# Optimization experiments

Hardware: AMD Instinct MI355X
Metric: run time of the kernel (lower is better)

Reference implementation:

```python
import jax, jax.numpy as jnp
import numpy as np

B, N, DIM, H, DH = 2, 2048, 1024, 16, 64
INNER = H * DH
ROPE_BASE = 10000.0


def setup_inputs() -> dict:
    key = jax.random.key(0)
    ks = jax.random.split(key, 6)
    s = 0.02
    return {
        "x": jax.random.normal(ks[0], (B, N, DIM), jnp.float32),
        "Wq": jax.random.normal(ks[1], (DIM, INNER), jnp.float32) * s,
        "Wk": jax.random.normal(ks[2], (DIM, INNER), jnp.float32) * s,
        "Wv": jax.random.normal(ks[3], (DIM, INNER), jnp.float32) * s,
        "Wo": jax.random.normal(ks[4], (INNER, DIM), jnp.float32) * s,
        "bo": jnp.zeros((DIM,), jnp.float32),
    }


def _rotate_half(x):
    # einops '... (d r) -> ... d r' with r=2: x1 = even lanes, x2 = odd lanes,
    # then cat((-x2, x1), dim=-1)
    x1 = x[..., 0::2]
    x2 = x[..., 1::2]
    return jnp.concatenate([-x2, x1], axis=-1)


def _rope_sin_cos(n, d, dtype):
    # inv_freq over arange(0, d, 2); emb = cat(f, f) -> length d
    inv_freq = 1.0 / (ROPE_BASE ** (jnp.arange(0, d, 2, dtype=jnp.float32) / d))
    f = jnp.arange(n, dtype=jnp.float32)[:, None] * inv_freq[None, :]  # [n, d/2]
    e = jnp.concatenate([f, f], axis=-1)  # [n, d]
    return jnp.sin(e).astype(dtype), jnp.cos(e).astype(dtype)


def _apply_rope(t, sin, cos):
    # t: [b, h, n, d]; sin/cos: [n, d]; rot_dim == d (full head), t_pass empty
    return t * cos[None, None] + _rotate_half(t) * sin[None, None]


def reference(x, Wq, Wk, Wv, Wo, bo):
    b, n, _ = x.shape
    scale = DH ** (-0.5)

    def split_heads(y):  # [b, n, h*d] -> [b, h, n, d]
        return y.reshape(b, n, H, DH).transpose(0, 2, 1, 3)

    q = split_heads(x @ Wq)
    k = split_heads(x @ Wk)
    v = split_heads(x @ Wv)

    sin, cos = _rope_sin_cos(n, DH, x.dtype)
    q = _apply_rope(q, sin, cos)
    k = _apply_rope(k, sin, cos)

    # causal SDPA (mask=None path -> is_causal=True), eval mode so dropout_p=0
    scores = jnp.einsum("bhqd,bhkd->bhqk", q, k) * scale
    causal = jnp.tril(jnp.ones((n, n), dtype=bool))
    scores = jnp.where(causal[None, None], scores, jnp.finfo(scores.dtype).min)
    probs = jax.nn.softmax(scores, axis=-1)
    attn = jnp.einsum("bhqk,bhkd->bhqd", probs, v)

    out = attn.transpose(0, 2, 1, 3).reshape(b, n, INNER) @ Wo + bo
    return out, k, v
```

## Files before the change

kernel.cpp:

```cpp
#include <hip/hip_runtime.h>
#include <cstdint>
#include <cmath>

#define BB   2
#define NN   2048
#define DIMM 1024
#define NHH  16
#define DHH  64
#define MMR  (BB * NN)

typedef _Float16 half8  __attribute__((ext_vector_type(8)));
typedef _Float16 half4v __attribute__((ext_vector_type(4)));
typedef float    f32x4  __attribute__((ext_vector_type(4)));

#define GLD16(gp, lp)                                                          \
  __builtin_amdgcn_global_load_lds(                                            \
      (const __attribute__((address_space(1))) unsigned int*)(gp),             \
      (__attribute__((address_space(3))) unsigned int*)(lp), 16, 0, 0)

__global__ __launch_bounds__(256) void cvt_x_kernel(const float* __restrict__ x,
                                                    _Float16* __restrict__ xh) {
  int i = (blockIdx.x * 256 + threadIdx.x) * 4;
  float4 v = *(const float4*)(x + i);
  half4v h;
  h[0] = (_Float16)v.x; h[1] = (_Float16)v.y;
  h[2] = (_Float16)v.z; h[3] = (_Float16)v.w;
  *(half4v*)(xh + i) = h;
}

__global__ __launch_bounds__(256) void transpose_w_kernel(
    const float* __restrict__ Wq, const float* __restrict__ Wk,
    const float* __restrict__ Wv, const float* __restrict__ Wo,
    _Float16* __restrict__ wt) {
  __shared__ float tile[64][65];
  int z = blockIdx.z;
  const float* W = (z == 0) ? Wq : (z == 1) ? Wk : (z == 2) ? Wv : Wo;
  _Float16* dst = wt + (size_t)z * 1024 * 1024;
  int r0 = blockIdx.x * 64;
  int c0 = blockIdx.y * 64;
  int t = threadIdx.x;
  int tr = t >> 4;
  int tc = (t & 15) * 4;
#pragma unroll
  for (int i = 0; i < 4; ++i) {
    float4 v = *(const float4*)(W + (size_t)(r0 + tr + i * 16) * 1024 + c0 + tc);
    tile[tr + i * 16][tc + 0] = v.x;
    tile[tr + i * 16][tc + 1] = v.y;
    tile[tr + i * 16][tc + 2] = v.z;
    tile[tr + i * 16][tc + 3] = v.w;
  }
  __syncthreads();
#pragma unroll
  for (int i = 0; i < 4; ++i) {
    int nl = tr + i * 16;
    half4v hv;
    hv[0] = (_Float16)tile[tc + 0][nl];
    hv[1] = (_Float16)tile[tc + 1][nl];
    hv[2] = (_Float16)tile[tc + 2][nl];
    hv[3] = (_Float16)tile[tc + 3][nl];
    *(half4v*)(dst + (size_t)(c0 + nl) * 1024 + r0 + tc) = hv;
  }
}

__global__ __launch_bounds__(256) void gemm_qkv_kernel(
    const _Float16* __restrict__ xh, const _Float16* __restrict__ wt,
    float* __restrict__ ko, float* __restrict__ vo,
    _Float16* __restrict__ qh, _Float16* __restrict__ kh,
    _Float16* __restrict__ vth) {
  __shared__ __align__(16) char smem[49152];
  _Float16* As = (_Float16*)smem;
  _Float16* Bs = (_Float16*)(smem + 24576);
  float (*Cs)[65] = (float(*)[65])smem;

  const int m0  = blockIdx.x * 64;
  const int ngl = blockIdx.y * 64;
  const int mat = ngl >> 10;
  const int n0  = ngl & 1023;
  const _Float16* wb = wt + (size_t)mat * 1024 * 1024;
  const int t = threadIdx.x;
  const int wv = t >> 6, lane = t & 63, l16 = lane & 15, quad = lane >> 4;
  const int r  = t >> 3;
  const int cl = t & 7;
  const int csw = (cl ^ (r & 7)) * 8;
  const _Float16* pa0 = xh + (size_t)(m0 + r) * 1024 + csw;
  const _Float16* pa1 = pa0 + 32 * 1024;
  const _Float16* pb0 = wb + (size_t)(n0 + r) * 1024 + csw;
  const _Float16* pb1 = pb0 + 32 * 1024;
  f32x4 acc[4] = {};
  const int arow = wv * 16 + l16;
  const int a7 = arow & 7;

#define STAGE_AB(k0s, nb) do {                                                 \
    GLD16(pa0 + (k0s), As + (nb) * 4096 + wv * 512);                           \
    GLD16(pa1 + (k0s), As + (nb) * 4096 + 2048 + wv * 512);                    \
    GLD16(pb0 + (k0s), Bs + (nb) * 4096 + wv * 512);                           \
    GLD16(pb1 + (k0s), Bs + (nb) * 4096 + 2048 + wv * 512);                    \
  } while (0)

  STAGE_AB(0, 0);
  STAGE_AB(64, 1);
  int cur = 0;
  for (int k0 = 0; k0 < 1024; k0 += 64) {
    if (k0 + 128 < 1024) {
      int nb = cur + 2; if (nb >= 3) nb -= 3;
      STAGE_AB(k0 + 128, nb);
      asm volatile("s_waitcnt vmcnt(8)" ::: "memory");
    } else if (k0 + 64 < 1024) {
      asm volatile("s_waitcnt vmcnt(4)" ::: "memory");
    } else {
      asm volatile("s_waitcnt vmcnt(0)" ::: "memory");
    }
    __builtin_amdgcn_s_barrier();
    asm volatile("" ::: "memory");
    const _Float16* Ab = As + cur * 4096;
    const _Float16* Bb = Bs + cur * 4096;
    half8 af0 = *(const half8*)(Ab + arow * 64 + (quad ^ a7) * 8);
    half8 af1 = *(const half8*)(Ab + arow * 64 + ((4 + quad) ^ a7) * 8);
#pragma unroll
    for (int nt = 0; nt < 4; ++nt) {
      int brow = nt * 16 + l16;
      int b7 = brow & 7;
      half8 bf0 = *(const half8*)(Bb + brow * 64 + (quad ^ b7) * 8);
      half8 bf1 = *(const half8*)(Bb + brow * 64 + ((4 + quad) ^ b7) * 8);
      acc[nt] = __builtin_amdgcn_mfma_f32_16x16x32_f16(af0, bf0, acc[nt], 0, 0, 0);
      acc[nt] = __builtin_amdgcn_mfma_f32_16x16x32_f16(af1, bf1, acc[nt], 0, 0, 0);
    }
    asm volatile("s_waitcnt lgkmcnt(0)" ::: "memory");
    __builtin_amdgcn_s_barrier();
    asm volatile("" ::: "memory");
    cur = (cur == 2) ? 0 : cur + 1;
  }
#undef STAGE_AB
#pragma unroll
  for (int nt = 0; nt < 4; ++nt)
#pragma unroll
    for (int rr = 0; rr < 4; ++rr)
      Cs[wv * 16 + quad * 4 + rr][nt * 16 + l16] = acc[nt][rr];
  __syncthreads();
  int lr = t >> 2;
  int cseg = (t & 3) * 16;
  int m = m0 + lr;
  int b = m >> 11;
  int pos = m & 2047;
  int h = n0 >> 6;
  int bhh = b * NHH + h;
  float vals[16];
  if (mat == 2) {
#pragma unroll
    for (int j = 0; j < 16; ++j) vals[j] = Cs[lr][cseg + j];
  } else {
    float fpos = (float)pos;
#pragma unroll
    for (int j = 0; j < 16; ++j) {
      int i = cseg + j;
      int jd = (i < 32) ? i : (i - 32);
      float invf = exp2f((float)jd * -0.41524101186092029f);
      float ang = fpos * invf;
      float sv, cv;
      sincosf(ang, &sv, &cv);
      float partner = (i < 32) ? -Cs[lr][2 * i + 1] : Cs[lr][2 * (i - 32)];
      vals[j] = Cs[lr][i] * cv + partner * sv;
    }
  }
  size_t rowb = ((size_t)bhh * NN + pos) * DHH + cseg;
  if (mat == 0) {
    half8 h0, h1;
#pragma unroll
    for (int j = 0; j < 8; ++j) { h0[j] = (_Float16)(vals[j] * 0.125f); h1[j] = (_Float16)(vals[8 + j] * 0.125f); }
    *(half8*)(qh + rowb) = h0;
    *(half8*)(qh + rowb + 8) = h1;
  } else if (mat == 1) {
#pragma unroll
    for (int j4 = 0; j4 < 4; ++j4) {
      float4 o;
      o.x = vals[j4 * 4 + 0]; o.y = vals[j4 * 4 + 1];
      o.z = vals[j4 * 4 + 2]; o.w = vals[j4 * 4 + 3];
      *(float4*)(ko + rowb + j4 * 4) = o;
    }
    half8 h0, h1;
#pragma unroll
    for (int j = 0; j < 8; ++j) { h0[j] = (_Float16)vals[j]; h1[j] = (_Float16)vals[8 + j]; }
    *(half8*)(kh + rowb) = h0;
    *(half8*)(kh + rowb + 8) = h1;
  } else {
#pragma unroll
    for (int j4 = 0; j4 < 4; ++j4) {
      float4 o;
      o.x = vals[j4 * 4 + 0]; o.y = vals[j4 * 4 + 1];
      o.z = vals[j4 * 4 + 2]; o.w = vals[j4 * 4 + 3];
      *(float4*)(vo + rowb + j4 * 4) = o;
    }
#pragma unroll
    for (int j = 0; j < 16; ++j)
      vth[((size_t)bhh * DHH + cseg + j) * NN + pos] = (_Float16)vals[j];
  }
}

__global__ __launch_bounds__(512) void fattn_kernel(
    const _Float16* __restrict__ qh, const _Float16* __restrict__ kh,
    const _Float16* __restrict__ vth, _Float16* __restrict__ ah) {
  __shared__ __align__(16) _Float16 Kt[3][4096];
  __shared__ __align__(16) _Float16 Vt[3][4096];
  __shared__ __align__(16) _Float16 Pb[8][16][72];
  const int lin  = (int)blockIdx.x;
  const int xcd  = lin & 7;
  const int slot = lin >> 3;
  const int bh   = xcd * 4 + (slot & 3);
  const int pair = slot >> 2;
  const int t = threadIdx.x;
  const int wv = t >> 6, lane = t & 63, l16 = lane & 15, quad = lane >> 4;
  const int b = bh >> 4, h = bh & 15;
  const _Float16* kg = kh + (size_t)bh * NN * DHH;
  const _Float16* vg = vth + (size_t)bh * DHH * NN;
  const int srow = t >> 3;
  const int sc   = ((t & 7) ^ (srow & 7)) * 8;
  half8 ones;
#pragma unroll
  for (int j = 0; j < 8; ++j) ones[j] = (_Float16)1.f;

#define STAGE_KV(tile, nb) do {                                                \
    const _Float16* kn_ = kg + (size_t)(tile) * 64 * DHH;                      \
    const _Float16* vn_ = vg + (tile) * 64;                                    \
    GLD16(kn_ + (size_t)srow * DHH + sc, &Kt[nb][0] + (wv * 64) * 8);          \
    GLD16(vn_ + (size_t)srow * NN + sc, &Vt[nb][0] + (wv * 64) * 8);           \
  } while (0)

  for (int job = 0; job < 2; ++job) {
    const int qb = (job == 0) ? (15 - pair) : pair;
    const int q0 = qb * 128;
    const int base = q0 + wv * 16;
    half8 qf0, qf1;
    {
      const _Float16* qp =
          qh + ((size_t)bh * NN + base + l16) * DHH + quad * 8;
      qf0 = *(const half8*)qp;
      qf1 = *(const half8*)(qp + 32);
    }
    f32x4 o[4] = {};
    f32x4 ls = {};
    const int ktmax = 2 * qb + 1;
    STAGE_KV(0, 0);
    STAGE_KV(1, 1);
    int cur = 0;
    for (int kt = 0; kt <= ktmax; ++kt) {
      if (kt + 2 <= ktmax) {
        int nb = cur + 2; if (nb >= 3) nb -= 3;
        STAGE_KV(kt + 2, nb);
        asm volatile("s_waitcnt vmcnt(4)" ::: "memory");
      } else if (kt + 1 <= ktmax) {
        asm volatile("s_waitcnt vmcnt(2)" ::: "memory");
      } else {
        asm volatile("s_waitcnt vmcnt(0)" ::: "memory");
      }
      __builtin_amdgcn_s_barrier();
      asm volatile("" ::: "memory");
      if (kt * 64 <= base + 15) {
        half8 kf[4][2], vf[4][2];
        const _Float16* Kb = &Kt[cur][0];
        const _Float16* Vb = &Vt[cur][0];
#pragma unroll
        for (int nt = 0; nt < 4; ++nt) {
          int row = nt * 16 + l16;
          int r7 = row & 7;
          kf[nt][0] = *(const half8*)(Kb + row * 64 + ((quad ^ r7) * 8));
          kf[nt][1] = *(const half8*)(Kb + row * 64 + (((quad + 4) ^ r7) * 8));
          vf[nt][0] = *(const half8*)(Vb + row * 64 + ((quad ^ r7) * 8));
          vf[nt][1] = *(const half8*)(Vb + row * 64 + (((quad + 4) ^ r7) * 8));
        }
        f32x4 s4[4];
#pragma unroll
        for (int nt = 0; nt < 4; ++nt) {
          f32x4 z = {};
          z = __builtin_amdgcn_mfma_f32_16x16x32_f16(qf0, kf[nt][0], z, 0, 0, 0);
          s4[nt] = __builtin_amdgcn_mfma_f32_16x16x32_f16(qf1, kf[nt][1], z, 0, 0, 0);
        }
        if (kt * 64 + 63 > base) {
#pragma unroll
          for (int nt = 0; nt < 4; ++nt) {
            int key = kt * 64 + nt * 16 + l16;
#pragma unroll
            for (int r = 0; r < 4; ++r) {
              float p = (key > base + quad * 4 + r) ? 0.f : __expf(s4[nt][r]);
              Pb[wv][quad * 4 + r][nt * 16 + l16] = (_Float16)p;
            }
          }
        } else {
#pragma unroll
          for (int nt = 0; nt < 4; ++nt)
#pragma unroll
            for (int r = 0; r < 4; ++r)
              Pb[wv][quad * 4 + r][nt * 16 + l16] = (_Float16)__expf(s4[nt][r]);
        }
        asm volatile("s_waitcnt lgkmcnt(0)" ::: "memory");
        half8 pf0 = *(const half8*)&Pb[wv][l16][quad * 8];
        half8 pf1 = *(const half8*)&Pb[wv][l16][32 + quad * 8];
#pragma unroll
        for (int nt = 0; nt < 4; ++nt) {
          o[nt] = __builtin_amdgcn_mfma_f32_16x16x32_f16(pf0, vf[nt][0], o[nt], 0, 0, 0);
          o[nt] = __builtin_amdgcn_mfma_f32_16x16x32_f16(pf1, vf[nt][1], o[nt], 0, 0, 0);
        }
        ls = __builtin_amdgcn_mfma_f32_16x16x32_f16(pf0, ones, ls, 0, 0, 0);
        ls = __builtin_amdgcn_mfma_f32_16x16x32_f16(pf1, ones, ls, 0, 0, 0);
      }
      asm volatile("s_waitcnt lgkmcnt(0)" ::: "memory");
      __builtin_amdgcn_s_barrier();
      asm volatile("" ::: "memory");
      cur = (cur == 2) ? 0 : cur + 1;
    }
#pragma unroll
    for (int r = 0; r < 4; ++r) {
      float inv = 1.f / ls[r];
      int pos = base + quad * 4 + r;
      size_t ob = ((size_t)(b * NN + pos)) * DIMM + h * DHH;
#pragma unroll
      for (int nt = 0; nt < 4; ++nt)
        ah[ob + nt * 16 + l16] = (_Float16)(o[nt][r] * inv);
    }
  }
#undef STAGE_KV
}

__global__ __launch_bounds__(256) void gemm_out_kernel(
    const _Float16* __restrict__ ah, const _Float16* __restrict__ wot,
    const float* __restrict__ bo, float* __restrict__ out) {
  __shared__ __align__(16) char smem[49152];
  _Float16* As = (_Float16*)smem;
  _Float16* Bs = (_Float16*)(smem + 24576);
  const int m0 = blockIdx.x * 64;
  const int n0 = blockIdx.y * 64;
  const int t = threadIdx.x;
  const int wv = t >> 6, lane = t & 63, l16 = lane & 15, quad = lane >> 4;
  const int r  = t >> 3;
  const int cl = t & 7;
  const int csw = (cl ^ (r & 7)) * 8;
  const _Float16* pa0 = ah + (size_t)(m0 + r) * 1024 + csw;
  const _Float16* pa1 = pa0 + 32 * 1024;
  const _Float16* pb0 = wot + (size_t)(n0 + r) * 1024 + csw;
  const _Float16* pb1 = pb0 + 32 * 1024;
  f32x4 acc[4] = {};
  const int arow = wv * 16 + l16;
  const int a7 = arow & 7;

#define STAGE_AB(k0s, nb) do {                                                 \
    GLD16(pa0 + (k0s), As + (nb) * 4096 + wv * 512);                           \
    GLD16(pa1 + (k0s), As + (nb) * 4096 + 2048 + wv * 512);                    \
    GLD16(pb0 + (k0s), Bs + (nb) * 4096 + wv * 512);                           \
    GLD16(pb1 + (k0s), Bs + (nb) * 4096 + 2048 + wv * 512);                    \
  } while (0)

  STAGE_AB(0, 0);
  STAGE_AB(64, 1);
  int cur = 0;
  for (int k0 = 0; k0 < 1024; k0 += 64) {
    if (k0 + 128 < 1024) {
      int nb = cur + 2; if (nb >= 3) nb -= 3;
      STAGE_AB(k0 + 128, nb);
      asm volatile("s_waitcnt vmcnt(8)" ::: "memory");
    } else if (k0 + 64 < 1024) {
      asm volatile("s_waitcnt vmcnt(4)" ::: "memory");
    } else {
      asm volatile("s_waitcnt vmcnt(0)" ::: "memory");
    }
    __builtin_amdgcn_s_barrier();
    asm volatile("" ::: "memory");
    const _Float16* Ab = As + cur * 4096;
    const _Float16* Bb = Bs + cur * 4096;
    half8 af0 = *(const half8*)(Ab + arow * 64 + (quad ^ a7) * 8);
    half8 af1 = *(const half8*)(Ab + arow * 64 + ((4 + quad) ^ a7) * 8);
#pragma unroll
    for (int nt = 0; nt < 4; ++nt) {
      int brow = nt * 16 + l16;
      int b7 = brow & 7;
      half8 bf0 = *(const half8*)(Bb + brow * 64 + (quad ^ b7) * 8);
      half8 bf1 = *(const half8*)(Bb + brow * 64 + ((4 + quad) ^ b7) * 8);
      acc[nt] = __builtin_amdgcn_mfma_f32_16x16x32_f16(af0, bf0, acc[nt], 0, 0, 0);
      acc[nt] = __builtin_amdgcn_mfma_f32_16x16x32_f16(af1, bf1, acc[nt], 0, 0, 0);
    }
    asm volatile("s_waitcnt lgkmcnt(0)" ::: "memory");
    __builtin_amdgcn_s_barrier();
    asm volatile("" ::: "memory");
    cur = (cur == 2) ? 0 : cur + 1;
  }
#undef STAGE_AB
#pragma unroll
  for (int nt = 0; nt < 4; ++nt) {
    int col = n0 + nt * 16 + l16;
    float bias = bo[col];
#pragma unroll
    for (int rr = 0; rr < 4; ++rr) {
      out[(size_t)(m0 + wv * 16 + quad * 4 + rr) * 1024 + col] = acc[nt][rr] + bias;
    }
  }
}

extern "C" void kernel_launch(void* const* d_in, const int* in_sizes, int n_in,
                              void* d_out, int out_size, void* d_ws, size_t ws_size,
                              hipStream_t stream) {
  (void)in_sizes; (void)n_in; (void)out_size; (void)ws_size;
  const float* x  = (const float*)d_in[0];
  const float* Wq = (const float*)d_in[1];
  const float* Wk = (const float*)d_in[2];
  const float* Wv = (const float*)d_in[3];
  const float* Wo = (const float*)d_in[4];
  const float* bo = (const float*)d_in[5];

  float* out = (float*)d_out;
  float* ko  = out + (size_t)MMR * DIMM;
  float* vo  = ko + (size_t)BB * NHH * NN * DHH;

  char* w = (char*)d_ws;
  _Float16* xh  = (_Float16*)w;
  _Float16* ah  = (_Float16*)w;
  _Float16* wt  = (_Float16*)(w + (8u << 20));
  _Float16* qh  = (_Float16*)(w + (16u << 20));
  _Float16* kh  = (_Float16*)(w + (24u << 20));
  _Float16* vth = (_Float16*)(w + (32u << 20));

  hipLaunchKernelGGL(cvt_x_kernel, dim3(4096), dim3(256), 0, stream, x, xh);
  hipLaunchKernelGGL(transpose_w_kernel, dim3(16, 16, 4), dim3(256), 0, stream,
                     Wq, Wk, Wv, Wo, wt);
  hipLaunchKernelGGL(gemm_qkv_kernel, dim3(64, 48), dim3(256), 0, stream,
                     xh, wt, ko, vo, qh, kh, vth);
  hipLaunchKernelGGL(fattn_kernel, dim3(256), dim3(512), 0, stream,
                     qh, kh, vth, ah);
  hipLaunchKernelGGL(gemm_out_kernel, dim3(64, 16), dim3(256), 0, stream,
                     ah, wt + (size_t)3 * 1024 * 1024, bo, out);
}
```

Before: 212.4 us.

## Enlarge QKV GEMM tile to 128x128 with double-buffered K=32 stages

The QKV projection GEMM moves from 64x64 tiles with a triple buffer at K=64 to 128x128 tiles where each wave computes a 64x64 sub-tile (4x4 MFMAs) over double-buffered K=32 stages with a new LDS swizzle. This raises arithmetic intensity per LDS load and halves global traffic for the operand tiles. The epilogue now writes two heads per block through a reused Cs buffer. The output GEMM drops from a triple to a double buffer to cut LDS use. The larger tiles leave only 768 blocks and raise register pressure, and the shallower pipeline exposes more load latency.

```diff
diff --git a/kernel.cpp b/kernel.cpp
--- a/kernel.cpp
+++ b/kernel.cpp
@@ -67,45 +67,49 @@
     float* __restrict__ ko, float* __restrict__ vo,
     _Float16* __restrict__ qh, _Float16* __restrict__ kh,
     _Float16* __restrict__ vth) {
-  __shared__ __align__(16) char smem[49152];
+  __shared__ __align__(16) char smem[33280];
   _Float16* As = (_Float16*)smem;
-  _Float16* Bs = (_Float16*)(smem + 24576);
+  _Float16* Bs = (_Float16*)(smem + 16384);
   float (*Cs)[65] = (float(*)[65])smem;
 
-  const int m0  = blockIdx.x * 64;
-  const int ngl = blockIdx.y * 64;
+  const int m0  = blockIdx.x * 128;
+  const int ngl = (int)blockIdx.y * 128;
   const int mat = ngl >> 10;
   const int n0  = ngl & 1023;
   const _Float16* wb = wt + (size_t)mat * 1024 * 1024;
   const int t = threadIdx.x;
   const int wv = t >> 6, lane = t & 63, l16 = lane & 15, quad = lane >> 4;
-  const int r  = t >> 3;
-  const int cl = t & 7;
-  const int csw = (cl ^ (r & 7)) * 8;
-  const _Float16* pa0 = xh + (size_t)(m0 + r) * 1024 + csw;
-  const _Float16* pa1 = pa0 + 32 * 1024;
-  const _Float16* pb0 = wb + (size_t)(n0 + r) * 1024 + csw;
-  const _Float16* pb1 = pb0 + 32 * 1024;
-  f32x4 acc[4] = {};
-  const int arow = wv * 16 + l16;
-  const int a7 = arow & 7;
+  const int wr = wv >> 1, wc = wv & 1;
+  const int srow = wv * 32 + (lane >> 2);
+  const int sg   = ((lane & 3) ^ ((lane >> 3) & 3)) * 8;
+  const _Float16* pa0 = xh + (size_t)(m0 + srow) * 1024 + sg;
+  const _Float16* pb0 = wb + (size_t)(n0 + srow) * 1024 + sg;
+  f32x4 acc[4][4] = {};
+  const int ksl = (quad ^ ((l16 >> 1) & 3)) * 8;
+  int aoff[4], boff[4];
+#pragma unroll
+  for (int mi = 0; mi < 4; ++mi) {
+    int arow = wr * 64 + mi * 16 + l16;
+    aoff[mi] = arow * 32 + ksl;
+  }
+#pragma unroll
+  for (int nt = 0; nt < 4; ++nt) {
+    int brow = wc * 64 + nt * 16 + l16;
+    boff[nt] = brow * 32 + ksl;
+  }
 
 #define STAGE_AB(k0s, nb) do {                                                 \
-    GLD16(pa0 + (k0s), As + (nb) * 4096 + wv * 512);                           \
-    GLD16(pa1 + (k0s), As + (nb) * 4096 + 2048 + wv * 512);                    \
-    GLD16(pb0 + (k0s), Bs + (nb) * 4096 + wv * 512);                           \
-    GLD16(pb1 + (k0s), Bs + (nb) * 4096 + 2048 + wv * 512);                    \
+    GLD16(pa0 + (k0s), As + (nb) * 4096 + wv * 1024);                          \
+    GLD16(pa0 + 16384 + (k0s), As + (nb) * 4096 + wv * 1024 + 512);            \
+    GLD16(pb0 + (k0s), Bs + (nb) * 4096 + wv * 1024);                          \
+    GLD16(pb0 + 16384 + (k0s), Bs + (nb) * 4096 + wv * 1024 + 512);            \
   } while (0)
 
   STAGE_AB(0, 0);
-  STAGE_AB(64, 1);
   int cur = 0;
-  for (int k0 = 0; k0 < 1024; k0 += 64) {
-    if (k0 + 128 < 1024) {
-      int nb = cur + 2; if (nb >= 3) nb -= 3;
-      STAGE_AB(k0 + 128, nb);
-      asm volatile("s_waitcnt vmcnt(8)" ::: "memory");
-    } else if (k0 + 64 < 1024) {
+  for (int k0 = 0; k0 < 1024; k0 += 32) {
+    if (k0 + 32 < 1024) {
+      STAGE_AB(k0 + 32, cur ^ 1);
       asm volatile("s_waitcnt vmcnt(4)" ::: "memory");
     } else {
       asm volatile("s_waitcnt vmcnt(0)" ::: "memory");
@@ -114,85 +118,94 @@
     asm volatile("" ::: "memory");
     const _Float16* Ab = As + cur * 4096;
     const _Float16* Bb = Bs + cur * 4096;
-    half8 af0 = *(const half8*)(Ab + arow * 64 + (quad ^ a7) * 8);
-    half8 af1 = *(const half8*)(Ab + arow * 64 + ((4 + quad) ^ a7) * 8);
-#pragma unroll
-    for (int nt = 0; nt < 4; ++nt) {
-      int brow = nt * 16 + l16;
-      int b7 = brow & 7;
-      half8 bf0 = *(const half8*)(Bb + brow * 64 + (quad ^ b7) * 8);
-      half8 bf1 = *(const half8*)(Bb + brow * 64 + ((4 + quad) ^ b7) * 8);
-      acc[nt] = __builtin_amdgcn_mfma_f32_16x16x32_f16(af0, bf0, acc[nt], 0, 0, 0);
-      acc[nt] = __builtin_amdgcn_mfma_f32_16x16x32_f16(af1, bf1, acc[nt], 0, 0, 0);
-    }
+    half8 af[4], bf[4];
+#pragma unroll
+    for (int mi = 0; mi < 4; ++mi) af[mi] = *(const half8*)(Ab + aoff[mi]);
+#pragma unroll
+    for (int nt = 0; nt < 4; ++nt) bf[nt] = *(const half8*)(Bb + boff[nt]);
+#pragma unroll
+    for (int mi = 0; mi < 4; ++mi)
+#pragma unroll
+      for (int nt = 0; nt < 4; ++nt)
+        acc[mi][nt] = __builtin_amdgcn_mfma_f32_16x16x32_f16(af[mi], bf[nt], acc[mi][nt], 0, 0, 0);
     asm volatile("s_waitcnt lgkmcnt(0)" ::: "memory");
     __builtin_amdgcn_s_barrier();
     asm volatile("" ::: "memory");
-    cur = (cur == 2) ? 0 : cur + 1;
+    cur ^= 1;
   }
 #undef STAGE_AB
-#pragma unroll
-  for (int nt = 0; nt < 4; ++nt)
-#pragma unroll
-    for (int rr = 0; rr < 4; ++rr)
-      Cs[wv * 16 + quad * 4 + rr][nt * 16 + l16] = acc[nt][rr];
-  __syncthreads();
-  int lr = t >> 2;
-  int cseg = (t & 3) * 16;
-  int m = m0 + lr;
-  int b = m >> 11;
-  int pos = m & 2047;
-  int h = n0 >> 6;
-  int bhh = b * NHH + h;
-  float vals[16];
-  if (mat == 2) {
-#pragma unroll
-    for (int j = 0; j < 16; ++j) vals[j] = Cs[lr][cseg + j];
-  } else {
-    float fpos = (float)pos;
-#pragma unroll
-    for (int j = 0; j < 16; ++j) {
-      int i = cseg + j;
-      int jd = (i < 32) ? i : (i - 32);
-      float invf = exp2f((float)jd * -0.41524101186092029f);
-      float ang = fpos * invf;
-      float sv, cv;
-      sincosf(ang, &sv, &cv);
-      float partner = (i < 32) ? -Cs[lr][2 * i + 1] : Cs[lr][2 * (i - 32)];
-      vals[j] = Cs[lr][i] * cv + partner * sv;
-    }
-  }
-  size_t rowb = ((size_t)bhh * NN + pos) * DHH + cseg;
-  if (mat == 0) {
-    half8 h0, h1;
-#pragma unroll
-    for (int j = 0; j < 8; ++j) { h0[j] = (_Float16)(vals[j] * 0.125f); h1[j] = (_Float16)(vals[8 + j] * 0.125f); }
-    *(half8*)(qh + rowb) = h0;
-    *(half8*)(qh + rowb + 8) = h1;
-  } else if (mat == 1) {
-#pragma unroll
-    for (int j4 = 0; j4 < 4; ++j4) {
-      float4 o;
-      o.x = vals[j4 * 4 + 0]; o.y = vals[j4 * 4 + 1];
-      o.z = vals[j4 * 4 + 2]; o.w = vals[j4 * 4 + 3];
-      *(float4*)(ko + rowb + j4 * 4) = o;
-    }
-    half8 h0, h1;
-#pragma unroll
-    for (int j = 0; j < 8; ++j) { h0[j] = (_Float16)vals[j]; h1[j] = (_Float16)vals[8 + j]; }
-    *(half8*)(kh + rowb) = h0;
-    *(half8*)(kh + rowb + 8) = h1;
-  } else {
-#pragma unroll
-    for (int j4 = 0; j4 < 4; ++j4) {
-      float4 o;
-      o.x = vals[j4 * 4 + 0]; o.y = vals[j4 * 4 + 1];
-      o.z = vals[j4 * 4 + 2]; o.w = vals[j4 * 4 + 3];
-      *(float4*)(vo + rowb + j4 * 4) = o;
-    }
-#pragma unroll
-    for (int j = 0; j < 16; ++j)
-      vth[((size_t)bhh * DHH + cseg + j) * NN + pos] = (_Float16)vals[j];
+  const int lr = t >> 1;
+  const int cseg = (t & 1) * 32;
+  const int m = m0 + lr;
+  const int b = m >> 11;
+  const int pos = m & 2047;
+  const float fpos = (float)pos;
+  for (int ch = 0; ch < 2; ++ch) {
+    __syncthreads();
+    if (wc == ch) {
+#pragma unroll
+      for (int mi = 0; mi < 4; ++mi)
+#pragma unroll
+        for (int nt = 0; nt < 4; ++nt)
+#pragma unroll
+          for (int rr = 0; rr < 4; ++rr)
+            Cs[wr * 64 + mi * 16 + quad * 4 + rr][nt * 16 + l16] = acc[mi][nt][rr];
+    }
+    __syncthreads();
+    const int h = (n0 >> 6) + ch;
+    const int bhh = b * NHH + h;
+    float vals[32];
+    if (mat == 2) {
+#pragma unroll
+      for (int j = 0; j < 32; ++j) vals[j] = Cs[lr][cseg + j];
+    } else {
+      const bool lo = (cseg == 0);
+#pragma unroll
+      for (int j = 0; j < 32; ++j) {
+        float invf = exp2f((float)j * -0.41524101186092029f);
+        float ang = fpos * invf;
+        float sv, cv;
+        sincosf(ang, &sv, &cv);
+        float partner = lo ? -Cs[lr][2 * j + 1] : Cs[lr][2 * j];
+        vals[j] = Cs[lr][cseg + j] * cv + partner * sv;
+      }
+    }
+    size_t rowb = ((size_t)bhh * NN + pos) * DHH + cseg;
+    if (mat == 0) {
+#pragma unroll
+      for (int j8 = 0; j8 < 4; ++j8) {
+        half8 hv;
+#pragma unroll
+        for (int j = 0; j < 8; ++j) hv[j] = (_Float16)(vals[j8 * 8 + j] * 0.125f);
+        *(half8*)(qh + rowb + j8 * 8) = hv;
+      }
+    } else if (mat == 1) {
+#pragma unroll
+      for (int j4 = 0; j4 < 8; ++j4) {
+        float4 o;
+        o.x = vals[j4 * 4 + 0]; o.y = vals[j4 * 4 + 1];
+        o.z = vals[j4 * 4 + 2]; o.w = vals[j4 * 4 + 3];
+        *(float4*)(ko + rowb + j4 * 4) = o;
+      }
+#pragma unroll
+      for (int j8 = 0; j8 < 4; ++j8) {
+        half8 hv;
+#pragma unroll
+        for (int j = 0; j < 8; ++j) hv[j] = (_Float16)vals[j8 * 8 + j];
+        *(half8*)(kh + rowb + j8 * 8) = hv;
+      }
+    } else {
+#pragma unroll
+      for (int j4 = 0; j4 < 8; ++j4) {
+        float4 o;
+        o.x = vals[j4 * 4 + 0]; o.y = vals[j4 * 4 + 1];
+        o.z = vals[j4 * 4 + 2]; o.w = vals[j4 * 4 + 3];
+        *(float4*)(vo + rowb + j4 * 4) = o;
+      }
+#pragma unroll
+      for (int j = 0; j < 32; ++j)
+        vth[((size_t)bhh * DHH + cseg + j) * NN + pos] = (_Float16)vals[j];
+    }
   }
 }
 
@@ -323,9 +336,9 @@
 __global__ __launch_bounds__(256) void gemm_out_kernel(
     const _Float16* __restrict__ ah, const _Float16* __restrict__ wot,
     const float* __restrict__ bo, float* __restrict__ out) {
-  __shared__ __align__(16) char smem[49152];
+  __shared__ __align__(16) char smem[32768];
   _Float16* As = (_Float16*)smem;
-  _Float16* Bs = (_Float16*)(smem + 24576);
+  _Float16* Bs = (_Float16*)(smem + 16384);
   const int m0 = blockIdx.x * 64;
   const int n0 = blockIdx.y * 64;
   const int t = threadIdx.x;
@@ -340,23 +353,18 @@
   f32x4 acc[4] = {};
   const int arow = wv * 16 + l16;
   const int a7 = arow & 7;
-
-#define STAGE_AB(k0s, nb) do {                                                 \
-    GLD16(pa0 + (k0s), As + (nb) * 4096 + wv * 512);                           \
-    GLD16(pa1 + (k0s), As + (nb) * 4096 + 2048 + wv * 512);                    \
-    GLD16(pb0 + (k0s), Bs + (nb) * 4096 + wv * 512);                           \
-    GLD16(pb1 + (k0s), Bs + (nb) * 4096 + 2048 + wv * 512);                    \
-  } while (0)
-
-  STAGE_AB(0, 0);
-  STAGE_AB(64, 1);
+  GLD16(pa0, As + wv * 512);
+  GLD16(pa1, As + 2048 + wv * 512);
+  GLD16(pb0, Bs + wv * 512);
+  GLD16(pb1, Bs + 2048 + wv * 512);
   int cur = 0;
   for (int k0 = 0; k0 < 1024; k0 += 64) {
-    if (k0 + 128 < 1024) {
-      int nb = cur + 2; if (nb >= 3) nb -= 3;
-      STAGE_AB(k0 + 128, nb);
-      asm volatile("s_waitcnt vmcnt(8)" ::: "memory");
-    } else if (k0 + 64 < 1024) {
+    if (k0 + 64 < 1024) {
+      const int nb = cur ^ 1;
+      GLD16(pa0 + k0 + 64, As + nb * 4096 + wv * 512);
+      GLD16(pa1 + k0 + 64, As + nb * 4096 + 2048 + wv * 512);
+      GLD16(pb0 + k0 + 64, Bs + nb * 4096 + wv * 512);
+      GLD16(pb1 + k0 + 64, Bs + nb * 4096 + 2048 + wv * 512);
       asm volatile("s_waitcnt vmcnt(4)" ::: "memory");
     } else {
       asm volatile("s_waitcnt vmcnt(0)" ::: "memory");
@@ -379,9 +387,8 @@
     asm volatile("s_waitcnt lgkmcnt(0)" ::: "memory");
     __builtin_amdgcn_s_barrier();
     asm volatile("" ::: "memory");
-    cur = (cur == 2) ? 0 : cur + 1;
-  }
-#undef STAGE_AB
+    cur ^= 1;
+  }
 #pragma unroll
   for (int nt = 0; nt < 4; ++nt) {
     int col = n0 + nt * 16 + l16;
@@ -419,7 +426,7 @@
   hipLaunchKernelGGL(cvt_x_kernel, dim3(4096), dim3(256), 0, stream, x, xh);
   hipLaunchKernelGGL(transpose_w_kernel, dim3(16, 16, 4), dim3(256), 0, stream,
                      Wq, Wk, Wv, Wo, wt);
-  hipLaunchKernelGGL(gemm_qkv_kernel, dim3(64, 48), dim3(256), 0, stream,
+  hipLaunchKernelGGL(gemm_qkv_kernel, dim3(32, 24), dim3(256), 0, stream,
                      xh, wt, ko, vo, qh, kh, vth);
   hipLaunchKernelGGL(fattn_kernel, dim3(256), dim3(512), 0, stream,
                      qh, kh, vth, ah);
```

New measurement: 233.1 us. +9.8%, slower.
